# Kernel tuning notes

Measured on AMD Instinct MI355X. Metric: run time of the kernel, lower is better.

The kernel has to match this reference:

```python
import jax, jax.numpy as jnp
import numpy as np

B, EMB, ARRAY = 4096, 512, 2
KW = KH = KC = 8
OC = 16                      # output_channel per branch
RED = OC * 2                 # SE hidden width
NUM_REL = 500
FC_IN = 3 * OC * KH * KW * KC  # 24576, flattened concat of 3 branches


def _make_chequer_perm():
    # Deterministic replication of MSLE.get_chequer_perm (perm=1).
    rng = np.random.RandomState(0)
    ent_perm = rng.permutation(EMB * (ARRAY - 1))
    rel_perm = rng.permutation(EMB)
    idxs, ei, ri = [], 0, 0
    for i in range(KC):
        for j in range(KH):
            for k in range(KW):
                for m in range(ARRAY):
                    if (i + j) % ARRAY == m:
                        idxs.append(int(rel_perm[ri]) + EMB * (ARRAY - 1)); ri += 1
                    else:
                        idxs.append(int(ent_perm[ei])); ei += 1
    return jnp.asarray(np.asarray(idxs, dtype=np.int32))


def setup_inputs() -> dict:
    key = jax.random.key(0)
    ks = jax.random.split(key, 12)
    n = lambda k, shape, s=0.05: jax.random.normal(k, shape, jnp.float32) * s
    f1_dim = ARRAY * OC * 1 * 1 * ARRAY        # (1,1,2) kernels
    f3_dim = ARRAY * OC * 1 * ARRAY * ARRAY    # (1,2,2) kernels
    f5_dim = ARRAY * OC * ARRAY * ARRAY * ARRAY  # (2,2,2) kernels
    z = lambda shape: jnp.zeros(shape, jnp.float32)
    o = lambda shape: jnp.ones(shape, jnp.float32)
    return {
        "concat_input": jax.random.normal(ks[0], (B, EMB * ARRAY), jnp.float32),
        "rel": jax.random.randint(ks[1], (B,), 0, NUM_REL),
        "chequer_perm": _make_chequer_perm(),
        "f1_table": n(ks[2], (NUM_REL, f1_dim)),
        "f3_table": n(ks[3], (NUM_REL, f3_dim)),
        "f5_table": n(ks[4], (NUM_REL, f5_dim)),
        "bn0_g": o((ARRAY,)), "bn0_b": z((ARRAY,)),
        "bn1_g": o((OC,)), "bn1_b": z((OC,)),
        "bn2_g": o((OC,)), "bn2_b": z((OC,)),
        "bn3_g": o((OC,)), "bn3_b": z((OC,)),
        "att_Wsq": n(ks[5], (OC, RED)), "att_bsq": z((RED,)),
        "att_W1": n(ks[6], (RED, OC)), "att_b1": z((OC,)),
        "att_W2": n(ks[7], (RED, OC)), "att_b2": z((OC,)),
        "att_W3": n(ks[8], (RED, OC)), "att_b3": z((OC,)),
        "fc_W": n(ks[9], (FC_IN, EMB), 0.01), "fc_b": z((EMB,)),
    }


def _bn(x, g, b, eps=1e-5):
    # BatchNorm3d, training-mode batch statistics over (N, D, H, W).
    m = x.mean(axis=(0, 2, 3, 4), keepdims=True)
    v = x.var(axis=(0, 2, 3, 4), keepdims=True)
    sh = (1, -1, 1, 1, 1)
    return (x - m) * jax.lax.rsqrt(v + eps) * g.reshape(sh) + b.reshape(sh)


def _per_sample_conv(x, w):
    # x: (B, Cin, D, H, W); w: (B, Cout, Cin, kd, kh, kw). 'same' padding,
    # even kernels pad the extra element at the high end (torch padding='same').
    conv1 = lambda xb, wb: jax.lax.conv_general_dilated(
        xb[None], wb, (1, 1, 1), 'SAME',
        dimension_numbers=('NCDHW', 'OIDHW', 'NCDHW'))[0]
    return jax.vmap(conv1)(x, w)


def reference(concat_input, rel, chequer_perm, f1_table, f3_table, f5_table,
              bn0_g, bn0_b, bn1_g, bn1_b, bn2_g, bn2_b, bn3_g, bn3_b,
              att_Wsq, att_bsq, att_W1, att_b1, att_W2, att_b2, att_W3, att_b3,
              fc_W, fc_b):
    b = concat_input.shape[0]
    # Chequered interleave of entity / relation embedding dims.
    x = concat_input[:, chequer_perm].reshape(b, ARRAY, KW, KH, KC)
    x = _bn(x, bn0_g, bn0_b)  # dropout = identity (eval)
    # Per-sample dynamic filters from relation embeddings.
    f1 = f1_table[rel].reshape(b, OC, ARRAY, 1, 1, ARRAY)
    f3 = f3_table[rel].reshape(b, OC, ARRAY, 1, ARRAY, ARRAY)
    f5 = f5_table[rel].reshape(b, OC, ARRAY, ARRAY, ARRAY, ARRAY)
    x1 = _bn(_per_sample_conv(x, f1), bn1_g, bn1_b)
    x3 = _bn(_per_sample_conv(x, f3), bn2_g, bn2_b)
    x5 = _bn(_per_sample_conv(x, f5), bn3_g, bn3_b)
    xs = x1 + x3 + x5
    # SE-style 3D attention: global pool -> shared squeeze -> 3 sigmoid gates.
    pooled = xs.mean(axis=(2, 3, 4))                       # (B, OC)
    zq = jax.nn.relu(pooled @ att_Wsq + att_bsq)           # (B, RED)
    gate = lambda W, bb: jax.nn.sigmoid(zq @ W + bb)[:, :, None, None, None]
    x1 = x1 * gate(att_W1, att_b1)
    x3 = x3 * gate(att_W2, att_b2)
    x5 = x5 * gate(att_W3, att_b3)
    out = jax.nn.relu(jnp.concatenate([x1, x3, x5], axis=1))
    out = out.reshape(b, -1)                               # (B, FC_IN)
    return out @ fc_W + fc_b                               # (B, EMB)
```

## Files before the change

kernel.cpp:

```cpp
#include <hip/hip_runtime.h>
#include <hip/hip_bf16.h>
#include <stdint.h>

typedef short s16x8 __attribute__((ext_vector_type(8)));
typedef short s16x4 __attribute__((ext_vector_type(4)));
typedef float f32x4 __attribute__((ext_vector_type(4)));

#define NB 4096
#define KTOT 24576
#define NOUT 512
#define NCH 48

__device__ __forceinline__ short f2bf(float f){
  union { float f; uint32_t u; } x; x.f = f;
  uint32_t r = (x.u + 0x7FFFu + ((x.u >> 16) & 1u)) >> 16;
  return (short)r;
}
__device__ __forceinline__ float bf2f(short s){
  union { uint32_t u; float f; } x; x.u = ((uint32_t)(uint16_t)s) << 16;
  return x.f;
}
__device__ __forceinline__ short f2bf_fast(float x){
  union { __hip_bfloat16 h; short s; } c; c.h = __float2bfloat16(x); return c.s;
}

#define GLOAD16(g, l) __builtin_amdgcn_global_load_lds( \
  (const __attribute__((address_space(1))) void*)(g), \
  (__attribute__((address_space(3))) void*)(l), 16, 0, 0)

__global__ __launch_bounds__(256) void k_colmap(const int* __restrict__ perm,
                                                int* __restrict__ chmap,
                                                float* __restrict__ statf){
  int q = blockIdx.x * 256 + threadIdx.x;
  if (q < 1024) chmap[perm[q]] = q >> 9;
  if (blockIdx.x == 0 && threadIdx.x < 4) statf[threadIdx.x] = 0.f;
}

__global__ __launch_bounds__(256) void k_bn0(const float* __restrict__ concat,
                                             const int* __restrict__ chmap,
                                             float* __restrict__ statf){
  int t = threadIdx.x;
  const int ch = chmap[(blockIdx.x*256 + t) & 1023];
  float s0=0,q0=0,s1=0,q1=0;
  for (int idx = blockIdx.x*256 + t; idx < NB*1024; idx += 2048*256){
    float v = concat[idx];
    if (ch){ s1 += v; q1 += v*v; } else { s0 += v; q0 += v*v; }
  }
  #pragma unroll
  for (int m=1;m<64;m<<=1){
    s0 += __shfl_xor(s0,m); q0 += __shfl_xor(q0,m);
    s1 += __shfl_xor(s1,m); q1 += __shfl_xor(q1,m);
  }
  __shared__ float lb[4][4];
  int wid = t>>6, lane = t&63;
  if (lane==0){ lb[wid][0]=s0; lb[wid][1]=q0; lb[wid][2]=s1; lb[wid][3]=q1; }
  __syncthreads();
  if (t==0){
    float a0=0,a1=0,a2=0,a3=0;
    #pragma unroll
    for (int w=0;w<4;w++){ a0+=lb[w][0]; a1+=lb[w][1]; a2+=lb[w][2]; a3+=lb[w][3]; }
    atomicAdd(&statf[0],a0); atomicAdd(&statf[1],a1);
    atomicAdd(&statf[2],a2); atomicAdd(&statf[3],a3);
  }
}

__global__ __launch_bounds__(256) void k_wcast(const float* __restrict__ fcW,
                                               short* __restrict__ wT){
  __shared__ float tile[64][65];
  int bid = blockIdx.x;
  int kb = (bid % 384) * 64;
  int nb = (bid / 384) * 64;
  int t = threadIdx.x;
  #pragma unroll
  for (int i=0;i<16;i++){
    int r = i*4 + (t>>6), c = t & 63;
    tile[r][c] = fcW[(size_t)(kb + r)*NOUT + nb + c];
  }
  __syncthreads();
  #pragma unroll
  for (int i=0;i<16;i++){
    int n = i*4 + (t>>6), k = t & 63;
    wT[(size_t)(nb + n)*KTOT + kb + k] = f2bf(tile[k][n]);
  }
}

__global__ __launch_bounds__(256) void k_conv(
    const float* __restrict__ concat, const int* __restrict__ perm,
    const int* __restrict__ rel,
    const float* __restrict__ f1t, const float* __restrict__ f3t,
    const float* __restrict__ f5t,
    const float* __restrict__ statf,
    const float* __restrict__ bn0g, const float* __restrict__ bn0b,
    short* __restrict__ raw, float* __restrict__ psum, float* __restrict__ psq)
{
  const int b = blockIdx.x;
  const int t = threadIdx.x;
  __shared__ float xn[2*9*9*9];
  __shared__ float filt[448];
  for (int i=t;i<1458;i+=256) xn[i]=0.f;
  int r = rel[b];
  for (int i=t;i<448;i+=256){
    float v;
    if (i < 64)       v = f1t[r*64 + i];
    else if (i < 192) v = f3t[r*128 + (i-64)];
    else              v = f5t[r*256 + (i-192)];
    filt[i]=v;
  }
  __syncthreads();
  const float n0inv = 1.f/(4096.f*512.f);
  float m0 = statf[0]*n0inv, e0 = statf[1]*n0inv;
  float m1 = statf[2]*n0inv, e1 = statf[3]*n0inv;
  float sc0 = bn0g[0]*rsqrtf(e0-m0*m0+1e-5f), sh0 = bn0b[0]-m0*sc0;
  float sc1 = bn0g[1]*rsqrtf(e1-m1*m1+1e-5f), sh1 = bn0b[1]-m1*sc1;
  for (int q=t;q<1024;q+=256){
    int col = perm[q];
    float v = concat[(size_t)b*1024 + col];
    int ch = q>>9, s = q & 511;
    int d = s>>6, h=(s>>3)&7, w=s&7;
    xn[ch*729 + d*81 + h*9 + w] = ch ? v*sc1+sh1 : v*sc0+sh0;
  }
  __syncthreads();

  const int wid = t>>6, lane = t&63;
  const int d = lane>>3, h = lane&7;
  float r00[9], r01[9], r10[9], r11[9], r20[9], r21[9], r30[9], r31[9];
  #pragma unroll
  for (int w9=0;w9<9;w9++){
    int base0 = d*81 + h*9 + w9;
    int base1 = d*81 + (h+1)*9 + w9;
    int base2 = (d+1)*81 + h*9 + w9;
    int base3 = (d+1)*81 + (h+1)*9 + w9;
    r00[w9]=xn[base0];      r01[w9]=xn[729+base0];
    r10[w9]=xn[base1];      r11[w9]=xn[729+base1];
    r20[w9]=xn[base2];      r21[w9]=xn[729+base2];
    r30[w9]=xn[base3];      r31[w9]=xn[729+base3];
  }
  const size_t rawbase = (size_t)b*KTOT;

  auto finish = [&](int c, const float* v){
    float s=0,q=0;
    #pragma unroll
    for (int p=0;p<8;p++){ s += v[p]; q += v[p]*v[p]; }
    #pragma unroll
    for (int m=1;m<64;m<<=1){ s += __shfl_xor(s,m); q += __shfl_xor(q,m); }
    if (lane==0){ psum[c*NB+b]=s; psq[c*NB+b]=q; }
    s16x8 pk;
    #pragma unroll
    for (int p=0;p<8;p++) pk[p] = f2bf_fast(v[p]);
    *reinterpret_cast<s16x8*>(raw + rawbase + (size_t)c*512 + lane*8) = pk;
  };

  #pragma unroll
  for (int i=0;i<4;i++){
    int oc = wid + 4*i;
    float c0=filt[oc*4+0], c1=filt[oc*4+1], c2=filt[oc*4+2], c3=filt[oc*4+3];
    float v[8];
    #pragma unroll
    for (int p=0;p<8;p++)
      v[p] = c0*r00[p]+c1*r00[p+1]+c2*r01[p]+c3*r01[p+1];
    finish(oc, v);
  }
  #pragma unroll
  for (int i=0;i<4;i++){
    int oc = wid + 4*i;
    const float* cf = &filt[64 + oc*8];
    float v[8];
    #pragma unroll
    for (int p=0;p<8;p++)
      v[p] = cf[0]*r00[p]+cf[1]*r00[p+1]+cf[2]*r10[p]+cf[3]*r10[p+1]
           + cf[4]*r01[p]+cf[5]*r01[p+1]+cf[6]*r11[p]+cf[7]*r11[p+1];
    finish(16+oc, v);
  }
  #pragma unroll
  for (int i=0;i<4;i++){
    int oc = wid + 4*i;
    const float* cf = &filt[192 + oc*16];
    float v[8];
    #pragma unroll
    for (int p=0;p<8;p++)
      v[p] = cf[0]*r00[p] +cf[1]*r00[p+1] +cf[2]*r10[p] +cf[3]*r10[p+1]
           + cf[4]*r20[p] +cf[5]*r20[p+1] +cf[6]*r30[p] +cf[7]*r30[p+1]
           + cf[8]*r01[p] +cf[9]*r01[p+1] +cf[10]*r11[p]+cf[11]*r11[p+1]
           + cf[12]*r21[p]+cf[13]*r21[p+1]+cf[14]*r31[p]+cf[15]*r31[p+1];
    finish(32+oc, v);
  }
}

__global__ __launch_bounds__(256) void k_bnstats(
    const float* __restrict__ psum, const float* __restrict__ psq,
    const float* __restrict__ bn1g, const float* __restrict__ bn1b,
    const float* __restrict__ bn2g, const float* __restrict__ bn2b,
    const float* __restrict__ bn3g, const float* __restrict__ bn3b,
    float* __restrict__ statf)
{
  int c = blockIdx.x, t = threadIdx.x;
  float s=0,q=0;
  for (int b=t;b<NB;b+=256){ s += psum[c*NB+b]; q += psq[c*NB+b]; }
  #pragma unroll
  for (int m=1;m<64;m<<=1){ s += __shfl_xor(s,m); q += __shfl_xor(q,m); }
  __shared__ float lb[4][2];
  int wid = t>>6, lane = t&63;
  if (lane==0){ lb[wid][0]=s; lb[wid][1]=q; }
  __syncthreads();
  if (t==0){
    s = lb[0][0]+lb[1][0]+lb[2][0]+lb[3][0];
    q = lb[0][1]+lb[1][1]+lb[2][1]+lb[3][1];
    float n = 4096.f*512.f;
    float mean = s/n, var = q/n - mean*mean;
    const float* g  = c<16 ? bn1g : (c<32 ? bn2g : bn3g);
    const float* bb = c<16 ? bn1b : (c<32 ? bn2b : bn3b);
    int oc = c & 15;
    float sc = g[oc]*rsqrtf(var + 1e-5f);
    statf[16+c] = sc;
    statf[64+c] = bb[oc] - mean*sc;
  }
}

__global__ __launch_bounds__(256) void k_se(
    const float* __restrict__ psum, const float* __restrict__ statf,
    const float* __restrict__ Wsq, const float* __restrict__ bsq,
    const float* __restrict__ W1, const float* __restrict__ b1,
    const float* __restrict__ W2, const float* __restrict__ b2,
    const float* __restrict__ W3, const float* __restrict__ b3,
    float* __restrict__ gates)
{
  int b = blockIdx.x*256 + threadIdx.x;
  float pooled[16];
  #pragma unroll
  for (int oc=0;oc<16;oc++){
    float p = 0.f;
    #pragma unroll
    for (int br=0;br<3;br++){
      int c = br*16 + oc;
      p += psum[c*NB+b]*(1.f/512.f)*statf[16+c] + statf[64+c];
    }
    pooled[oc] = p;
  }
  float zq[32];
  #pragma unroll
  for (int r2=0;r2<32;r2++){
    float z = bsq[r2];
    #pragma unroll
    for (int oc=0;oc<16;oc++) z += pooled[oc]*Wsq[oc*32+r2];
    zq[r2] = fmaxf(z, 0.f);
  }
  #pragma unroll
  for (int br=0;br<3;br++){
    const float* W  = br==0 ? W1 : (br==1 ? W2 : W3);
    const float* bb = br==0 ? b1 : (br==1 ? b2 : b3);
    #pragma unroll
    for (int oc=0;oc<16;oc++){
      float g = bb[oc];
      #pragma unroll
      for (int r2=0;r2<32;r2++) g += zq[r2]*W[r2*16+oc];
      gates[(size_t)(br*16+oc)*NB + b] = 1.f/(1.f + expf(-g));
    }
  }
}

__global__ __launch_bounds__(512, 2) void k_gemm(
    const short* __restrict__ raw, const short* __restrict__ wT,
    const float* __restrict__ scale, const float* __restrict__ shift,
    const float* __restrict__ gates, short* __restrict__ partials)
{
  const int t = threadIdx.x;
  const int bid = blockIdx.x;
  const int sk = bid & 7, mblk = bid >> 3;
  const int b0 = mblk*128;
  const int kb0 = sk*3072;

  __shared__ __align__(16) short Al[5][128*32];
  __shared__ __align__(16) short Wl[3][512*32];
  __shared__ float gscL[6*128], gshL[6*128];

  const int wid = t>>6, lane = t&63;
  const int wm = wid>>2, wn = wid&3;
  const int fr = lane&15, kq = lane>>4;

  for (int i=t;i<768;i+=512){
    int c = i>>7, r = i&127;
    int ch = sk*6 + c;
    float g = gates[(size_t)ch*NB + b0 + r];
    gscL[i] = scale[ch]*g;
    gshL[i] = shift[ch]*g;
  }
  __syncthreads();

  const int row_t = wid*16 + (lane>>2);
  const int gsw = (((lane&3) ^ ((lane>>3)&3)))*8;
  const short* ap = raw + (size_t)(b0+row_t)*KTOT + kb0 + gsw;
  const short* wp0 = wT + (size_t)(wid*64 +  0 + (lane>>2))*KTOT + kb0 + gsw;
  const short* wp1 = wT + (size_t)(wid*64 + 16 + (lane>>2))*KTOT + kb0 + gsw;
  const short* wp2 = wT + (size_t)(wid*64 + 32 + (lane>>2))*KTOT + kb0 + gsw;
  const short* wp3 = wT + (size_t)(wid*64 + 48 + (lane>>2))*KTOT + kb0 + gsw;

  const int so16 = (kq ^ ((fr>>1)&3))<<4;
  int afb[4], bfb[8];
  #pragma unroll
  for (int m=0;m<4;m++) afb[m] = (wm*64 + m*16 + fr)*64 + so16;
  #pragma unroll
  for (int n=0;n<8;n++) bfb[n] = (wn*128 + n*16 + fr)*64 + so16;

  f32x4 acc[4][8];
  #pragma unroll
  for (int m=0;m<4;m++)
    #pragma unroll
    for (int n=0;n<8;n++){ f32x4 z = {0.f,0.f,0.f,0.f}; acc[m][n]=z; }

  #define STAGE_W(sl, ko_) { \
    GLOAD16(wp0 + (ko_), &Wl[sl][(wid*64 +  0)*32]); \
    GLOAD16(wp1 + (ko_), &Wl[sl][(wid*64 + 16)*32]); \
    GLOAD16(wp2 + (ko_), &Wl[sl][(wid*64 + 32)*32]); \
    GLOAD16(wp3 + (ko_), &Wl[sl][(wid*64 + 48)*32]); }
  #define STAGE_A(sl, ko_)  GLOAD16(ap + (ko_), &Al[sl][wid*512])

  #define XF(sl, tl) { \
    int ch_ = (tl)>>4; ch_ = ch_>5 ? 5 : ch_; \
    float sc_ = gscL[ch_*128 + row_t], sh_ = gshL[ch_*128 + row_t]; \
    short* p_ = &Al[sl][wid*512 + lane*8]; \
    s16x8 v_ = *reinterpret_cast<const s16x8*>(p_); \
    s16x8 o_; \
    _Pragma("unroll") \
    for (int j_=0;j_<8;j_++) o_[j_] = f2bf_fast(fmaxf(bf2f(v_[j_])*sc_+sh_, 0.f)); \
    *reinterpret_cast<s16x8*>(p_) = o_; }

  #define LGKM0 asm volatile("s_waitcnt lgkmcnt(0)" ::: "memory")

  STAGE_A(0, 0);  STAGE_A(1, 32);
  STAGE_W(0, 0);  STAGE_A(2, 64);
  STAGE_W(1, 32); STAGE_A(3, 96);
  asm volatile("s_waitcnt vmcnt(10)" ::: "memory");
  XF(0, 0);
  LGKM0;

  int sl_r = 0, sl_x = 1, sl_a = 4;
  int sw_r = 0, sw_s = 2;
  for (int s = 0; s < 96; ++s){
    asm volatile("s_waitcnt vmcnt(6)" ::: "memory");
    __builtin_amdgcn_s_barrier();
    __builtin_amdgcn_sched_barrier(0);
    STAGE_W(sw_s, (s+2)*32);
    STAGE_A(sl_a, (s+4)*32);
    const char* Ab = (const char*)Al[sl_r];
    const char* Wb = (const char*)Wl[sw_r];
    s16x8 af[4], bf[8];
    #pragma unroll
    for (int m=0;m<4;m++) af[m] = *reinterpret_cast<const s16x8*>(Ab + afb[m]);
    #pragma unroll
    for (int n=0;n<8;n++) bf[n] = *reinterpret_cast<const s16x8*>(Wb + bfb[n]);
    __builtin_amdgcn_s_setprio(1);
    #pragma unroll
    for (int m=0;m<4;m++)
      #pragma unroll
      for (int n=0;n<8;n++)
        acc[m][n] = __builtin_amdgcn_mfma_f32_16x16x32_bf16(af[m], bf[n], acc[m][n], 0,0,0);
    __builtin_amdgcn_s_setprio(0);
    XF(sl_x, s+1);
    LGKM0;
    sl_r = sl_x; sl_x = (sl_x==4)?0:sl_x+1; sl_a = (sl_a==4)?0:sl_a+1;
    sw_r = (sw_r==2)?0:sw_r+1; sw_s = (sw_s==2)?0:sw_s+1;
  }

  short* pb = partials + (size_t)sk*NB*NOUT;
  #pragma unroll
  for (int m=0;m<4;m++){
    #pragma unroll
    for (int j=0;j<4;j++){
      int row = b0 + wm*64 + m*16 + kq*4 + j;
      short* prow = pb + (size_t)row*NOUT + wn*128 + fr;
      #pragma unroll
      for (int n=0;n<8;n++) prow[n*16] = f2bf_fast(acc[m][n][j]);
    }
  }
  #undef STAGE_W
  #undef STAGE_A
  #undef XF
  #undef LGKM0
}

__global__ __launch_bounds__(256) void k_red(const short* __restrict__ partials,
                                             const float* __restrict__ fcb,
                                             float* __restrict__ out){
  int i = blockIdx.x*256 + threadIdx.x;
  int base = i*4;
  f32x4 v = *reinterpret_cast<const f32x4*>(fcb + (base & 511));
  #pragma unroll
  for (int sk=0;sk<8;sk++){
    s16x4 p = *reinterpret_cast<const s16x4*>(partials + (size_t)sk*2097152 + base);
    v[0] += bf2f(p[0]); v[1] += bf2f(p[1]);
    v[2] += bf2f(p[2]); v[3] += bf2f(p[3]);
  }
  *reinterpret_cast<f32x4*>(out + base) = v;
}

extern "C" void kernel_launch(void* const* d_in, const int* in_sizes, int n_in,
                              void* d_out, int out_size, void* d_ws, size_t ws_size,
                              hipStream_t stream) {
  const float* concat = (const float*)d_in[0];
  const int*   rel    = (const int*)  d_in[1];
  const int*   perm   = (const int*)  d_in[2];
  const float* f1t = (const float*)d_in[3];
  const float* f3t = (const float*)d_in[4];
  const float* f5t = (const float*)d_in[5];
  const float* bn0g=(const float*)d_in[6],  *bn0b=(const float*)d_in[7];
  const float* bn1g=(const float*)d_in[8],  *bn1b=(const float*)d_in[9];
  const float* bn2g=(const float*)d_in[10], *bn2b=(const float*)d_in[11];
  const float* bn3g=(const float*)d_in[12], *bn3b=(const float*)d_in[13];
  const float* Wsq=(const float*)d_in[14],  *bsq=(const float*)d_in[15];
  const float* W1=(const float*)d_in[16],   *b1=(const float*)d_in[17];
  const float* W2=(const float*)d_in[18],   *b2=(const float*)d_in[19];
  const float* W3=(const float*)d_in[20],   *b3=(const float*)d_in[21];
  const float* fcW=(const float*)d_in[22],  *fcb=(const float*)d_in[23];
  float* out = (float*)d_out;
  char* ws = (char*)d_ws;

  const size_t off_raw  = 0;
  const size_t off_wT   = 201326592;
  const size_t off_part = 226492416;
  const size_t off_psum = 260046848;
  const size_t off_psq  = 260833280;
  const size_t off_gate = 261619712;
  const size_t off_stat = 262406144;
  const size_t off_chm  = 262406656;
  const size_t need     = off_chm + 4096;
  if (ws_size < need) return;

  short* raw      = (short*)(ws + off_raw);
  short* wT       = (short*)(ws + off_wT);
  short* partials = (short*)(ws + off_part);
  float* psum     = (float*)(ws + off_psum);
  float* psq      = (float*)(ws + off_psq);
  float* gates    = (float*)(ws + off_gate);
  float* statf    = (float*)(ws + off_stat);
  int*   chmap    = (int*)  (ws + off_chm);

  k_colmap<<<4, 256, 0, stream>>>(perm, chmap, statf);
  k_bn0   <<<2048, 256, 0, stream>>>(concat, chmap, statf);
  k_wcast <<<3072, 256, 0, stream>>>(fcW, wT);
  k_conv  <<<4096, 256, 0, stream>>>(concat, perm, rel, f1t, f3t, f5t,
                                     statf, bn0g, bn0b, raw, psum, psq);
  k_bnstats<<<48, 256, 0, stream>>>(psum, psq, bn1g, bn1b, bn2g, bn2b,
                                    bn3g, bn3b, statf);
  k_se    <<<16, 256, 0, stream>>>(psum, statf, Wsq, bsq, W1, b1, W2, b2,
                                   W3, b3, gates);
  k_gemm  <<<256, 512, 0, stream>>>(raw, wT, statf+16, statf+64, gates, partials);
  k_red   <<<2048, 256, 0, stream>>>(partials, fcb, out);
}
```

Before: 422.2 us.

## Split GEMM main loop into two barrier-separated MFMA phases and reduce conv stats via LDS

The GEMM k-loop is restructured into two halves. Each half loads some B fragments, hits a barrier, then issues 16 MFMAs. The A-tile staging and the XF transform are moved between the halves so that memory and LDS work interleaves with matrix math across waves. Separately, the conv kernel's per-channel sum and square-sum reduction now uses three shuffles plus an LDS partial array finished by 48 threads, instead of a full 64-lane shuffle tree. This adds extra block barriers per iteration, which may cost synchronisation time.

```diff
diff --git a/kernel.cpp b/kernel.cpp
--- a/kernel.cpp
+++ b/kernel.cpp
@@ -97,6 +97,7 @@
   const int t = threadIdx.x;
   __shared__ float xn[2*9*9*9];
   __shared__ float filt[448];
+  __shared__ float redS[48][9], redQ[48][9];
   for (int i=t;i<1458;i+=256) xn[i]=0.f;
   int r = rel[b];
   for (int i=t;i<448;i+=256){
@@ -141,9 +142,10 @@
     float s=0,q=0;
     #pragma unroll
     for (int p=0;p<8;p++){ s += v[p]; q += v[p]*v[p]; }
-    #pragma unroll
-    for (int m=1;m<64;m<<=1){ s += __shfl_xor(s,m); q += __shfl_xor(q,m); }
-    if (lane==0){ psum[c*NB+b]=s; psq[c*NB+b]=q; }
+    s += __shfl_xor(s,1); q += __shfl_xor(q,1);
+    s += __shfl_xor(s,2); q += __shfl_xor(q,2);
+    s += __shfl_xor(s,4); q += __shfl_xor(q,4);
+    if ((lane&7)==0){ redS[c][lane>>3]=s; redQ[c][lane>>3]=q; }
     s16x8 pk;
     #pragma unroll
     for (int p=0;p<8;p++) pk[p] = f2bf_fast(v[p]);
@@ -183,6 +185,13 @@
            + cf[8]*r01[p] +cf[9]*r01[p+1] +cf[10]*r11[p]+cf[11]*r11[p+1]
            + cf[12]*r21[p]+cf[13]*r21[p+1]+cf[14]*r31[p]+cf[15]*r31[p+1];
     finish(32+oc, v);
+  }
+  __syncthreads();
+  if (t < 48){
+    float s=0,q=0;
+    #pragma unroll
+    for (int j=0;j<8;j++){ s += redS[t][j]; q += redQ[t][j]; }
+    psum[t*NB+b]=s; psq[t*NB+b]=q;
   }
 }
 
@@ -325,6 +334,8 @@
     *reinterpret_cast<s16x8*>(p_) = o_; }
 
   #define LGKM0 asm volatile("s_waitcnt lgkmcnt(0)" ::: "memory")
+  #define SCHED0 __builtin_amdgcn_sched_barrier(0)
+  #define BAR __builtin_amdgcn_s_barrier()
 
   STAGE_A(0, 0);  STAGE_A(1, 32);
   STAGE_W(0, 0);  STAGE_A(2, 64);
@@ -337,26 +348,40 @@
   int sw_r = 0, sw_s = 2;
   for (int s = 0; s < 96; ++s){
     asm volatile("s_waitcnt vmcnt(6)" ::: "memory");
-    __builtin_amdgcn_s_barrier();
-    __builtin_amdgcn_sched_barrier(0);
+    BAR;
+    SCHED0;
     STAGE_W(sw_s, (s+2)*32);
-    STAGE_A(sl_a, (s+4)*32);
     const char* Ab = (const char*)Al[sl_r];
     const char* Wb = (const char*)Wl[sw_r];
     s16x8 af[4], bf[8];
     #pragma unroll
     for (int m=0;m<4;m++) af[m] = *reinterpret_cast<const s16x8*>(Ab + afb[m]);
     #pragma unroll
-    for (int n=0;n<8;n++) bf[n] = *reinterpret_cast<const s16x8*>(Wb + bfb[n]);
+    for (int n=0;n<4;n++) bf[n] = *reinterpret_cast<const s16x8*>(Wb + bfb[n]);
+    BAR;
+    LGKM0; SCHED0;
     __builtin_amdgcn_s_setprio(1);
     #pragma unroll
     for (int m=0;m<4;m++)
       #pragma unroll
-      for (int n=0;n<8;n++)
+      for (int n=0;n<4;n++)
         acc[m][n] = __builtin_amdgcn_mfma_f32_16x16x32_bf16(af[m], bf[n], acc[m][n], 0,0,0);
     __builtin_amdgcn_s_setprio(0);
+    BAR;
+    SCHED0;
+    STAGE_A(sl_a, (s+4)*32);
+    #pragma unroll
+    for (int n=4;n<8;n++) bf[n] = *reinterpret_cast<const s16x8*>(Wb + bfb[n]);
     XF(sl_x, s+1);
-    LGKM0;
+    BAR;
+    LGKM0; SCHED0;
+    __builtin_amdgcn_s_setprio(1);
+    #pragma unroll
+    for (int m=0;m<4;m++)
+      #pragma unroll
+      for (int n=4;n<8;n++)
+        acc[m][n] = __builtin_amdgcn_mfma_f32_16x16x32_bf16(af[m], bf[n], acc[m][n], 0,0,0);
+    __builtin_amdgcn_s_setprio(0);
     sl_r = sl_x; sl_x = (sl_x==4)?0:sl_x+1; sl_a = (sl_a==4)?0:sl_a+1;
     sw_r = (sw_r==2)?0:sw_r+1; sw_s = (sw_s==2)?0:sw_s+1;
   }
@@ -376,6 +401,8 @@
   #undef STAGE_A
   #undef XF
   #undef LGKM0
+  #undef SCHED0
+  #undef BAR
 }
 
 __global__ __launch_bounds__(256) void k_red(const short* __restrict__ partials,
```

Result: slower. 447.1 us (+5.9%).
